# Performance work log

Measured on AMD Instinct MI355X. Metric: run time of the kernel, lower is better.

Reference implementation:

```python
import jax, jax.numpy as jnp
import numpy as np

NEG_SLOPE = 0.01  # torch F.leaky_relu default
N_USER = 100000
N_ITEM = 100000
N_EDGE = 640000
D = 128
N_LAYERS = 3  # 1 input + num_hidden_layers(1) + 1 output layer


def setup_inputs() -> dict:
    key = jax.random.key(0)
    ks = jax.random.split(key, 10)
    scale = 1.0 / np.sqrt(D)
    return {
        "h_user": jax.random.normal(ks[0], (N_USER, D), dtype=jnp.float32),
        "h_item": jax.random.normal(ks[1], (N_ITEM, D), dtype=jnp.float32),
        # W[layer, etype] : etype 0 = user-follows->user, 1 = user-clicks->item, 2 = item-clicked_by->user
        "W": jax.random.normal(ks[2], (N_LAYERS, 3, D, D), dtype=jnp.float32) * scale,
        "b": jnp.zeros((N_LAYERS, 3, D), dtype=jnp.float32),
        "follows_src": jax.random.randint(ks[3], (N_EDGE,), 0, N_USER, dtype=jnp.int32),
        "follows_dst": jax.random.randint(ks[4], (N_EDGE,), 0, N_USER, dtype=jnp.int32),
        "clicks_src": jax.random.randint(ks[5], (N_EDGE,), 0, N_USER, dtype=jnp.int32),
        "clicks_dst": jax.random.randint(ks[6], (N_EDGE,), 0, N_ITEM, dtype=jnp.int32),
        "cb_src": jax.random.randint(ks[7], (N_EDGE,), 0, N_ITEM, dtype=jnp.int32),
        "cb_dst": jax.random.randint(ks[8], (N_EDGE,), 0, N_USER, dtype=jnp.int32),
    }


def _etype_conv(h_src, W, b, src, dst, n_dst):
    """Per-etype Linear on src nodes, copy_u gather, mean-aggregate at dst."""
    Wh = h_src @ W + b                     # [N_src, D] dense transform (once per node)
    msg = Wh[src]                          # [E, D] gather
    s = jax.ops.segment_sum(msg, dst, num_segments=n_dst)
    cnt = jax.ops.segment_sum(jnp.ones((src.shape[0],), dtype=Wh.dtype), dst, num_segments=n_dst)
    return s / jnp.maximum(cnt, 1.0)[:, None]  # mean; isolated nodes -> 0


def _rgcn_forward(h_user, h_item, W, b, follows_src, follows_dst,
                  clicks_src, clicks_dst, cb_src, cb_dst):
    hu, hi = h_user, h_item
    for l in range(N_LAYERS):
        # per-etype mean aggregation, then cross-etype 'sum' (DGL multi_update_all)
        agg_u = (_etype_conv(hu, W[l, 0], b[l, 0], follows_src, follows_dst, N_USER)
                 + _etype_conv(hi, W[l, 2], b[l, 2], cb_src, cb_dst, N_USER))
        agg_i = _etype_conv(hu, W[l, 1], b[l, 1], clicks_src, clicks_dst, N_ITEM)
        hu = jax.nn.leaky_relu(agg_u, NEG_SLOPE)
        hi = jax.nn.leaky_relu(agg_i, NEG_SLOPE)
    return jnp.stack([hu, hi])  # [2, 100000, 128]


def reference(h_user, h_item, W, b, follows_src, follows_dst,
              clicks_src, clicks_dst, cb_src, cb_dst):
    return _rgcn_forward(h_user, h_item, W, b, follows_src, follows_dst,
                         clicks_src, clicks_dst, cb_src, cb_dst)
```

## Files before the change

### kernel.cpp

```cpp
#include <hip/hip_runtime.h>

typedef unsigned char u8;
typedef unsigned short u16;
typedef _Float16 f16;
typedef __attribute__((ext_vector_type(4))) _Float16 f16x4;
typedef __attribute__((ext_vector_type(8))) _Float16 f16x8;
typedef __attribute__((ext_vector_type(4))) float f32x4;

#define D 128
#define PG 4

__global__ __launch_bounds__(256) void k_pre(
    const float* __restrict__ h_user, const float* __restrict__ h_item,
    const float* __restrict__ W,
    const int* __restrict__ fd, const int* __restrict__ cd,
    const int* __restrict__ cbd,
    u16* __restrict__ h_all, u16* __restrict__ Wtg,
    int* __restrict__ cnt, u8* __restrict__ pos,
    int NU, int NI, int nf, int nc, int ncb,
    int nbCnt, int nbCvtU, int nbCvtI) {
  int b = blockIdx.x;
  int T = gridDim.x;
  long before = (long)b * nbCnt / T;
  long after = (long)(b + 1) * nbCnt / T;
  if (after > before) {
    int e = (int)before * 256 + threadIdx.x;
    int d;
    if (e < nf)
      d = fd[e];
    else if (e < nf + nc)
      d = NU + cd[e - nf];
    else if (e < nf + nc + ncb)
      d = NU + NI + cbd[e - nf - nc];
    else
      return;
    int p = atomicAdd(&cnt[d], 1);
    pos[e] = (u8)p;
  } else {
    int v = b - (int)before;
    if (v < nbCvtU + nbCvtI) {
      bool isU = v < nbCvtU;
      int i = (isU ? v : v - nbCvtU) * 256 + threadIdx.x;
      int n8 = (isU ? NU : NI) * 16;
      if (i >= n8) return;
      const float4* ip = (const float4*)(isU ? h_user : h_item);
      u16* op = h_all + (isU ? 0 : (size_t)NU * D);
      float4 a = ip[i * 2], c = ip[i * 2 + 1];
      f16x8 vv = {(f16)a.x, (f16)a.y, (f16)a.z, (f16)a.w,
                  (f16)c.x, (f16)c.y, (f16)c.z, (f16)c.w};
      *(f16x8*)(op + (size_t)i * 8) = vv;
    } else {
      int idx = (v - nbCvtU - nbCvtI) * 256 + threadIdx.x;
      if (idx >= 9 * 16384) return;
      int mat = idx >> 14;
      int k = (idx >> 7) & 127;
      int n = idx & 127;
      ((f16*)Wtg)[(size_t)mat * 16384 + n * 128 + k] = (f16)W[idx];
    }
  }
}

__device__ __forceinline__ int pad4(int x) { return (x + (PG - 1)) & ~(PG - 1); }

__global__ __launch_bounds__(256) void k_scanA(const int* __restrict__ cnt,
                                               int* __restrict__ part, int n) {
  int t = threadIdx.x;
  int idx = blockIdx.x * 1024 + t * 4;
  int s = 0;
  if (idx + 3 < n) {
    int4 c = *(const int4*)(cnt + idx);
    s = pad4(c.x) + pad4(c.y) + pad4(c.z) + pad4(c.w);
  } else {
#pragma unroll
    for (int j = 0; j < 4; ++j)
      if (idx + j < n) s += pad4(cnt[idx + j]);
  }
  for (int off = 1; off < 64; off <<= 1) s += __shfl_down(s, off, 64);
  __shared__ int ws[4];
  if ((t & 63) == 0) ws[t >> 6] = s;
  __syncthreads();
  if (t == 0) part[blockIdx.x] = ws[0] + ws[1] + ws[2] + ws[3];
}

__global__ __launch_bounds__(1024) void k_scanB(int* __restrict__ part, int n_part) {
  __shared__ int sh[1024];
  int t = threadIdx.x;
  int v = (t < n_part) ? part[t] : 0;
  sh[t] = v;
  __syncthreads();
  for (int off = 1; off < 1024; off <<= 1) {
    int u = (t >= off) ? sh[t - off] : 0;
    __syncthreads();
    sh[t] += u;
    __syncthreads();
  }
  if (t < n_part) part[t] = sh[t] - v;
}

__global__ __launch_bounds__(256) void k_scanC(const int* __restrict__ cnt,
                                               const int* __restrict__ part,
                                               int* __restrict__ rs, int n) {
  int t = threadIdx.x;
  int idx = blockIdx.x * 1024 + t * 4;
  int v0 = 0, v1 = 0, v2 = 0, v3 = 0;
  if (idx + 3 < n) {
    int4 c = *(const int4*)(cnt + idx);
    v0 = pad4(c.x);
    v1 = pad4(c.y);
    v2 = pad4(c.z);
    v3 = pad4(c.w);
  } else {
    if (idx < n) v0 = pad4(cnt[idx]);
    if (idx + 1 < n) v1 = pad4(cnt[idx + 1]);
    if (idx + 2 < n) v2 = pad4(cnt[idx + 2]);
    if (idx + 3 < n) v3 = pad4(cnt[idx + 3]);
  }
  int s = v0 + v1 + v2 + v3;
  int inc = s;
  int lane = t & 63, w = t >> 6;
  for (int off = 1; off < 64; off <<= 1) {
    int u = __shfl_up(inc, off, 64);
    if (lane >= off) inc += u;
  }
  __shared__ int ws[4];
  if (lane == 63) ws[w] = inc;
  __syncthreads();
  int woff = 0;
  for (int i = 0; i < w; ++i) woff += ws[i];
  int ex = part[blockIdx.x] + woff + inc - s;
  int4 r;
  r.x = ex;
  r.y = ex + v0;
  r.z = r.y + v1;
  r.w = r.z + v2;
  if (idx + 3 < n)
    *(int4*)(rs + idx) = r;
  else {
    if (idx < n) rs[idx] = r.x;
    if (idx + 1 < n) rs[idx + 1] = r.y;
    if (idx + 2 < n) rs[idx + 2] = r.z;
    if (idx + 3 < n) rs[idx + 3] = r.w;
  }
  if (idx <= n - 1 && n - 1 < idx + 4) {
    int j = n - 1 - idx;
    int incl = (j == 0) ? r.x + v0 : (j == 1) ? r.y + v1 : (j == 2) ? r.z + v2 : r.w + v3;
    rs[n] = incl;
  }
}

__global__ __launch_bounds__(256) void k_padfill(const int* __restrict__ rs,
                                                 const int* __restrict__ cnt,
                                                 int* __restrict__ csr, int N3, int ZR) {
  int d = blockIdx.x * 256 + threadIdx.x;
  if (d >= N3) return;
  int deg = cnt[d];
  int degp = pad4(deg);
  int base = rs[d] + deg;
#pragma unroll
  for (int j = 0; j < PG - 1; ++j)
    if (j < degp - deg) csr[base + j] = ZR;
}

__global__ __launch_bounds__(256) void k_fillpos(
    const int* __restrict__ fs, const int* __restrict__ fd,
    const int* __restrict__ cs, const int* __restrict__ cd,
    const int* __restrict__ cbs, const int* __restrict__ cbd,
    const int* __restrict__ rs, const u8* __restrict__ pos,
    int* __restrict__ csr, int NU, int NI, int nf, int nc, int ncb) {
  int e = blockIdx.x * 256 + threadIdx.x;
  int d, s;
  if (e < nf) {
    d = fd[e];
    s = fs[e];
  } else if (e < nf + nc) {
    d = NU + cd[e - nf];
    s = cs[e - nf];
  } else if (e < nf + nc + ncb) {
    d = NU + NI + cbd[e - nf - nc];
    s = cbs[e - nf - nc] + NU;
  } else
    return;
  csr[rs[d] + (int)pos[e]] = s;
}

__global__ __launch_bounds__(256) void k_agg3(
    const u16* __restrict__ h_all, const int* __restrict__ csr,
    const int* __restrict__ rs, const int* __restrict__ cnt,
    u16* __restrict__ M_all, int N3) {
  int wave = (blockIdx.x * 256 + threadIdx.x) >> 6;
  int lane = threadIdx.x & 63;
  int l16 = lane & 15;
  int w = wave * 4 + (lane >> 4);
  bool valid = w < N3;
  int wc = valid ? w : 0;
  int e = rs[wc];
  int en = valid ? rs[wc + 1] : e;
  int deg = valid ? cnt[wc] : 0;
  f16x8 acc0 = {0, 0, 0, 0, 0, 0, 0, 0};
  f16x8 acc1 = {0, 0, 0, 0, 0, 0, 0, 0};
  const char* hb = (const char*)h_all;
  unsigned loff = (unsigned)l16 * 16u;

  int en8 = e + ((en - e) & ~7);
  while (e < en8) {
    int s0 = csr[e], s1 = csr[e + 1], s2 = csr[e + 2], s3 = csr[e + 3];
    int s4 = csr[e + 4], s5 = csr[e + 5], s6 = csr[e + 6], s7 = csr[e + 7];
    f16x8 v0 = *(const f16x8*)(hb + ((unsigned)s0 * 256u + loff));
    f16x8 v1 = *(const f16x8*)(hb + ((unsigned)s1 * 256u + loff));
    f16x8 v2 = *(const f16x8*)(hb + ((unsigned)s2 * 256u + loff));
    f16x8 v3 = *(const f16x8*)(hb + ((unsigned)s3 * 256u + loff));
    f16x8 v4 = *(const f16x8*)(hb + ((unsigned)s4 * 256u + loff));
    f16x8 v5 = *(const f16x8*)(hb + ((unsigned)s5 * 256u + loff));
    f16x8 v6 = *(const f16x8*)(hb + ((unsigned)s6 * 256u + loff));
    f16x8 v7 = *(const f16x8*)(hb + ((unsigned)s7 * 256u + loff));
    acc0 += v0;
    acc1 += v1;
    acc0 += v2;
    acc1 += v3;
    acc0 += v4;
    acc1 += v5;
    acc0 += v6;
    acc1 += v7;
    e += 8;
  }
  if (e < en) {
    int s0 = csr[e], s1 = csr[e + 1], s2 = csr[e + 2], s3 = csr[e + 3];
    f16x8 v0 = *(const f16x8*)(hb + ((unsigned)s0 * 256u + loff));
    f16x8 v1 = *(const f16x8*)(hb + ((unsigned)s1 * 256u + loff));
    f16x8 v2 = *(const f16x8*)(hb + ((unsigned)s2 * 256u + loff));
    f16x8 v3 = *(const f16x8*)(hb + ((unsigned)s3 * 256u + loff));
    acc0 += v0;
    acc1 += v1;
    acc0 += v2;
    acc1 += v3;
  }

  if (valid) {
    float invf = deg > 0 ? 1.0f / (float)deg : 0.f;
    f16 hinv = (f16)invf;
    f16x8 t = acc0 + acc1;
    f16x8 r = t * hinv;
    *(f16x8*)((char*)M_all + ((unsigned)wc * 256u + loff)) = r;
  }
}

template <int NE, int OUTF32>
__device__ __forceinline__ void gemm_body(
    const u16* __restrict__ mA, const u16* __restrict__ mBp,
    const u16* __restrict__ wtA, const u16* __restrict__ wtB,
    const float* __restrict__ bA, const float* __restrict__ bB,
    const int* __restrict__ rsA, const int* __restrict__ rsB,
    u16* __restrict__ o16, float* __restrict__ o32, int M, int blk) {
  int tid = threadIdx.x, lane = tid & 63, w = tid >> 6;
  int lr = lane & 15;
  int lk = (lane >> 4) * 8;
  long row0 = (long)blk * 128 + w * 32;

  f32x4 acc[2][8];
#pragma unroll
  for (int rt = 0; rt < 2; rt++)
#pragma unroll
    for (int n = 0; n < 8; n++) acc[rt][n] = (f32x4){0.f, 0.f, 0.f, 0.f};

#pragma unroll
  for (int e = 0; e < NE; ++e) {
    const f16* mm = (const f16*)((e == 0) ? mA : mBp);
    const f16* Wg = (const f16*)((e == 0) ? wtA : wtB);
#pragma unroll
    for (int ks = 0; ks < 4; ++ks) {
      int k0 = ks * 32 + lk;
      f16x8 bf[8];
#pragma unroll
      for (int n = 0; n < 8; n++) bf[n] = *(const f16x8*)(Wg + (n * 16 + lr) * D + k0);
#pragma unroll
      for (int rt = 0; rt < 2; rt++) {
        long r = row0 + rt * 16 + lr;
        if (r >= M) r = M - 1;
        f16x8 af = *(const f16x8*)(mm + r * D + k0);
#pragma unroll
        for (int n = 0; n < 8; n++)
          acc[rt][n] = __builtin_amdgcn_mfma_f32_16x16x32_f16(bf[n], af, acc[rt][n], 0, 0, 0);
      }
    }
  }

  int g4 = (lane >> 4) * 4;
  float4 bAr[8], bBr[8];
#pragma unroll
  for (int n = 0; n < 8; n++) {
    bAr[n] = *(const float4*)&bA[n * 16 + g4];
    if (NE == 2) bBr[n] = *(const float4*)&bB[n * 16 + g4];
  }

#pragma unroll
  for (int rt = 0; rt < 2; rt++) {
    long r = row0 + rt * 16 + lr;
    if (r < M) {
      bool mAok = rsA[r + 1] > rsA[r];
      bool mBok = (NE == 2) && (rsB[r + 1] > rsB[r]);
#pragma unroll
      for (int n = 0; n < 8; n++) {
        float4 vv;
        vv.x = acc[rt][n][0];
        vv.y = acc[rt][n][1];
        vv.z = acc[rt][n][2];
        vv.w = acc[rt][n][3];
        if (mAok) {
          vv.x += bAr[n].x;
          vv.y += bAr[n].y;
          vv.z += bAr[n].z;
          vv.w += bAr[n].w;
        }
        if (mBok) {
          vv.x += bBr[n].x;
          vv.y += bBr[n].y;
          vv.z += bBr[n].z;
          vv.w += bBr[n].w;
        }
        vv.x = vv.x > 0.f ? vv.x : 0.01f * vv.x;
        vv.y = vv.y > 0.f ? vv.y : 0.01f * vv.y;
        vv.z = vv.z > 0.f ? vv.z : 0.01f * vv.z;
        vv.w = vv.w > 0.f ? vv.w : 0.01f * vv.w;
        int col = n * 16 + g4;
        if (OUTF32) {
          *(float4*)&o32[r * D + col] = vv;
        } else {
          f16x4 h = {(f16)vv.x, (f16)vv.y, (f16)vv.z, (f16)vv.w};
          *(f16x4*)((f16*)o16 + r * D + col) = h;
        }
      }
    }
  }
}

template <int OUTF32>
__global__ __launch_bounds__(256) void k_gemm2(
    const u16* __restrict__ M_all, const u16* __restrict__ Wl,
    const float* __restrict__ bl, const int* __restrict__ rs_all,
    u16* __restrict__ h_all, float* __restrict__ out,
    int NU, int NI, int nbI) {
  if ((int)blockIdx.x < nbI) {
    gemm_body<1, OUTF32>(M_all + (size_t)NU * D, nullptr,
                         Wl + 16384, nullptr,
                         bl + D, nullptr,
                         rs_all + NU, nullptr,
                         h_all + (size_t)NU * D, out + (size_t)NU * D, NI,
                         blockIdx.x);
  } else {
    gemm_body<2, OUTF32>(M_all, M_all + (size_t)(NU + NI) * D,
                         Wl, Wl + 2 * 16384,
                         bl, bl + 2 * D,
                         rs_all, rs_all + NU + NI,
                         h_all, out, NU, blockIdx.x - nbI);
  }
}

extern "C" void kernel_launch(void* const* d_in, const int* in_sizes, int n_in,
                              void* d_out, int out_size, void* d_ws, size_t ws_size,
                              hipStream_t stream) {
  const float* h_user = (const float*)d_in[0];
  const float* h_item = (const float*)d_in[1];
  const float* W = (const float*)d_in[2];
  const float* bb = (const float*)d_in[3];
  const int* f_src = (const int*)d_in[4];
  const int* f_dst = (const int*)d_in[5];
  const int* c_src = (const int*)d_in[6];
  const int* c_dst = (const int*)d_in[7];
  const int* cb_src = (const int*)d_in[8];
  const int* cb_dst = (const int*)d_in[9];

  const int NU = in_sizes[0] / D;
  const int NI = in_sizes[1] / D;
  const int nEf = in_sizes[4], nEc = in_sizes[6], nEcb = in_sizes[8];
  const int N3 = NU + NI + NU;
  const int nE = nEf + nEc + nEcb;
  const int ZR = NU + NI;

  char* p = (char*)d_ws;
  auto alloc = [&](size_t bytes) {
    char* r = p;
    p += (bytes + 255) & ~(size_t)255;
    return r;
  };
  int* cnt = (int*)alloc((size_t)N3 * 4);
  int* rs_all = (int*)alloc((size_t)(N3 + 1) * 4);
  int* part = (int*)alloc(1024 * 4);
  u16* Wtg = (u16*)alloc((size_t)9 * 16384 * 2);
  int* csr_all = (int*)alloc(((size_t)nE + (size_t)(PG - 1) * N3) * 4);
  u16* h_all = (u16*)alloc((size_t)(NU + NI + 1) * D * 2);
  u16* M_all = (u16*)alloc((size_t)N3 * D * 2);
  u8* pos = (u8*)M_all;
  (void)ws_size;

  hipMemsetAsync(cnt, 0, (size_t)N3 * 4, stream);
  hipMemsetAsync(h_all + (size_t)ZR * D, 0, D * 2, stream);

  int nbCnt = (nE + 255) / 256;
  int nbCvtU = (NU * 16 + 255) / 256;
  int nbCvtI = (NI * 16 + 255) / 256;
  int nbW = (9 * 16384 + 255) / 256;
  k_pre<<<nbCnt + nbCvtU + nbCvtI + nbW, 256, 0, stream>>>(
      h_user, h_item, W, f_dst, c_dst, cb_dst, h_all, Wtg, cnt, pos,
      NU, NI, nEf, nEc, nEcb, nbCnt, nbCvtU, nbCvtI);

  int n_part = (N3 + 1023) / 1024;
  k_scanA<<<n_part, 256, 0, stream>>>(cnt, part, N3);
  k_scanB<<<1, 1024, 0, stream>>>(part, n_part);
  k_scanC<<<n_part, 256, 0, stream>>>(cnt, part, rs_all, N3);

  k_padfill<<<(N3 + 255) / 256, 256, 0, stream>>>(rs_all, cnt, csr_all, N3, ZR);
  k_fillpos<<<(nE + 255) / 256, 256, 0, stream>>>(f_src, f_dst, c_src, c_dst,
                                                  cb_src, cb_dst, rs_all, pos,
                                                  csr_all, NU, NI, nEf, nEc, nEcb);

  int nbI = (NI + 127) / 128;
  int nbU = (NU + 127) / 128;
  int agg_blocks = ((N3 + 3) / 4 + 3) / 4;

  for (int l = 0; l < 3; ++l) {
    const u16* Wl = Wtg + (size_t)l * 3 * 16384;
    const float* bl = bb + (size_t)l * 3 * D;

    k_agg3<<<agg_blocks, 256, 0, stream>>>(h_all, csr_all, rs_all, cnt, M_all, N3);

    if (l < 2)
      k_gemm2<0><<<nbI + nbU, 256, 0, stream>>>(M_all, Wl, bl, rs_all, h_all,
                                                (float*)d_out, NU, NI, nbI);
    else
      k_gemm2<1><<<nbI + nbU, 256, 0, stream>>>(M_all, Wl, bl, rs_all, h_all,
                                                (float*)d_out, NU, NI, nbI);
  }
}
```

Baseline: 549.2 us.

## Fuse neighbor aggregation and per-etype GEMM into one layer kernel

Replaces the separate aggregation kernel and GEMM kernel with a single per-layer kernel. Each wave gathers and mean-reduces neighbor rows for 16 destination nodes straight into MFMA A-fragments, then multiplies by the weights, so the fp16 M_all intermediate is never written or read back. The gathered features and the next layer's output now need separate buffers, so ping-pong h buffers are added. The cost is lower gather parallelism per node, since 16 nodes share a wave and divergent degrees are handled with a __any loop padded to the zero row, plus weights being re-read per wave without reuse across rows.

New measurement: 688.0 us. 1.25x slower.

```diff
diff --git a/kernel.cpp b/kernel.cpp
--- a/kernel.cpp
+++ b/kernel.cpp
@@ -183,175 +183,141 @@
   csr[rs[d] + (int)pos[e]] = s;
 }
 
-__global__ __launch_bounds__(256) void k_agg3(
-    const u16* __restrict__ h_all, const int* __restrict__ csr,
-    const int* __restrict__ rs, const int* __restrict__ cnt,
-    u16* __restrict__ M_all, int N3) {
-  int wave = (blockIdx.x * 256 + threadIdx.x) >> 6;
+__device__ __forceinline__ int gather_frag(
+    f16x8 a[4], const char* __restrict__ hb, const int* __restrict__ csr,
+    const int* __restrict__ rs, const int* __restrict__ cnt, int gnode, int ZR) {
   int lane = threadIdx.x & 63;
-  int l16 = lane & 15;
-  int w = wave * 4 + (lane >> 4);
-  bool valid = w < N3;
-  int wc = valid ? w : 0;
-  int e = rs[wc];
-  int en = valid ? rs[wc + 1] : e;
-  int deg = valid ? cnt[wc] : 0;
-  f16x8 acc0 = {0, 0, 0, 0, 0, 0, 0, 0};
-  f16x8 acc1 = {0, 0, 0, 0, 0, 0, 0, 0};
-  const char* hb = (const char*)h_all;
-  unsigned loff = (unsigned)l16 * 16u;
-
-  int en8 = e + ((en - e) & ~7);
-  while (e < en8) {
-    int s0 = csr[e], s1 = csr[e + 1], s2 = csr[e + 2], s3 = csr[e + 3];
-    int s4 = csr[e + 4], s5 = csr[e + 5], s6 = csr[e + 6], s7 = csr[e + 7];
-    f16x8 v0 = *(const f16x8*)(hb + ((unsigned)s0 * 256u + loff));
-    f16x8 v1 = *(const f16x8*)(hb + ((unsigned)s1 * 256u + loff));
-    f16x8 v2 = *(const f16x8*)(hb + ((unsigned)s2 * 256u + loff));
-    f16x8 v3 = *(const f16x8*)(hb + ((unsigned)s3 * 256u + loff));
-    f16x8 v4 = *(const f16x8*)(hb + ((unsigned)s4 * 256u + loff));
-    f16x8 v5 = *(const f16x8*)(hb + ((unsigned)s5 * 256u + loff));
-    f16x8 v6 = *(const f16x8*)(hb + ((unsigned)s6 * 256u + loff));
-    f16x8 v7 = *(const f16x8*)(hb + ((unsigned)s7 * 256u + loff));
-    acc0 += v0;
-    acc1 += v1;
-    acc0 += v2;
-    acc1 += v3;
-    acc0 += v4;
-    acc1 += v5;
-    acc0 += v6;
-    acc1 += v7;
-    e += 8;
-  }
-  if (e < en) {
-    int s0 = csr[e], s1 = csr[e + 1], s2 = csr[e + 2], s3 = csr[e + 3];
-    f16x8 v0 = *(const f16x8*)(hb + ((unsigned)s0 * 256u + loff));
-    f16x8 v1 = *(const f16x8*)(hb + ((unsigned)s1 * 256u + loff));
-    f16x8 v2 = *(const f16x8*)(hb + ((unsigned)s2 * 256u + loff));
-    f16x8 v3 = *(const f16x8*)(hb + ((unsigned)s3 * 256u + loff));
-    acc0 += v0;
-    acc1 += v1;
-    acc0 += v2;
-    acc1 += v3;
-  }
-
+  int g = lane >> 4;
+  int e = rs[gnode], en = rs[gnode + 1];
+  int deg = cnt[gnode];
+  unsigned off = (unsigned)g * 16u;
+  f16x8 a0 = {0, 0, 0, 0, 0, 0, 0, 0}, a1 = a0, a2 = a0, a3 = a0;
+  while (__any(e < en)) {
+    bool p = e < en;
+    int s0 = p ? csr[e] : ZR;
+    int s1 = p ? csr[e + 1] : ZR;
+    unsigned b0 = (unsigned)s0 * 256u + off;
+    unsigned b1 = (unsigned)s1 * 256u + off;
+    f16x8 v00 = *(const f16x8*)(hb + b0);
+    f16x8 v01 = *(const f16x8*)(hb + b0 + 64u);
+    f16x8 v02 = *(const f16x8*)(hb + b0 + 128u);
+    f16x8 v03 = *(const f16x8*)(hb + b0 + 192u);
+    f16x8 v10 = *(const f16x8*)(hb + b1);
+    f16x8 v11 = *(const f16x8*)(hb + b1 + 64u);
+    f16x8 v12 = *(const f16x8*)(hb + b1 + 128u);
+    f16x8 v13 = *(const f16x8*)(hb + b1 + 192u);
+    a0 += v00;
+    a1 += v01;
+    a2 += v02;
+    a3 += v03;
+    a0 += v10;
+    a1 += v11;
+    a2 += v12;
+    a3 += v13;
+    e += 2;
+  }
+  float invf = deg > 0 ? 1.0f / (float)deg : 0.f;
+  f16 hinv = (f16)invf;
+  a[0] = a0 * hinv;
+  a[1] = a1 * hinv;
+  a[2] = a2 * hinv;
+  a[3] = a3 * hinv;
+  return deg;
+}
+
+__device__ __forceinline__ void mfma_frag(f32x4 acc[8], const f16x8 a[4],
+                                          const u16* __restrict__ Wmat) {
+  int lane = threadIdx.x & 63;
+  int r = lane & 15, g = lane >> 4;
+  const f16* Wg = (const f16*)Wmat;
+#pragma unroll
+  for (int half = 0; half < 2; ++half) {
+#pragma unroll
+    for (int ks = 0; ks < 4; ++ks) {
+      f16x8 bf[4];
+#pragma unroll
+      for (int n4 = 0; n4 < 4; ++n4) {
+        int n = half * 4 + n4;
+        bf[n4] = *(const f16x8*)(Wg + (n * 16 + r) * D + ks * 32 + g * 8);
+      }
+#pragma unroll
+      for (int n4 = 0; n4 < 4; ++n4)
+        acc[half * 4 + n4] =
+            __builtin_amdgcn_mfma_f32_16x16x32_f16(bf[n4], a[ks], acc[half * 4 + n4], 0, 0, 0);
+    }
+  }
+}
+
+template <int OUTF32>
+__global__ __launch_bounds__(256) void k_layer(
+    const u16* __restrict__ hcur, const int* __restrict__ csr,
+    const int* __restrict__ rs_all, const int* __restrict__ cnt,
+    const u16* __restrict__ Wl, const float* __restrict__ bl,
+    u16* __restrict__ hnxt, float* __restrict__ out,
+    int NU, int NI, int nwI, int nwU, int ZR) {
+  int wid = blockIdx.x * 4 + (threadIdx.x >> 6);
+  if (wid >= nwI + nwU) return;
+  int lane = threadIdx.x & 63;
+  int r = lane & 15, g = lane >> 4;
+  const char* hb = (const char*)hcur;
+
+  bool isItem = wid < nwI;
+  int node = (isItem ? wid : wid - nwI) * 16 + r;
+  int Ntgt = isItem ? NI : NU;
+  bool valid = node < Ntgt;
+  int nodec = valid ? node : Ntgt - 1;
+
+  f32x4 acc[8];
+#pragma unroll
+  for (int n = 0; n < 8; ++n) acc[n] = (f32x4){0.f, 0.f, 0.f, 0.f};
+
+  f16x8 a[4];
+  int gA = isItem ? NU + nodec : nodec;
+  int degA = gather_frag(a, hb, csr, rs_all, cnt, gA, ZR);
+  mfma_frag(acc, a, isItem ? Wl + 16384 : Wl);
+  int degB = 0;
+  if (!isItem) {
+    degB = gather_frag(a, hb, csr, rs_all, cnt, NU + NI + nodec, ZR);
+    mfma_frag(acc, a, Wl + 2 * 16384);
+  }
+
+  const float* bA = isItem ? bl + D : bl;
+  long orow = (long)(isItem ? NU + node : node) * D;
+  bool mA = degA > 0, mB = degB > 0;
   if (valid) {
-    float invf = deg > 0 ? 1.0f / (float)deg : 0.f;
-    f16 hinv = (f16)invf;
-    f16x8 t = acc0 + acc1;
-    f16x8 r = t * hinv;
-    *(f16x8*)((char*)M_all + ((unsigned)wc * 256u + loff)) = r;
-  }
-}
-
-template <int NE, int OUTF32>
-__device__ __forceinline__ void gemm_body(
-    const u16* __restrict__ mA, const u16* __restrict__ mBp,
-    const u16* __restrict__ wtA, const u16* __restrict__ wtB,
-    const float* __restrict__ bA, const float* __restrict__ bB,
-    const int* __restrict__ rsA, const int* __restrict__ rsB,
-    u16* __restrict__ o16, float* __restrict__ o32, int M, int blk) {
-  int tid = threadIdx.x, lane = tid & 63, w = tid >> 6;
-  int lr = lane & 15;
-  int lk = (lane >> 4) * 8;
-  long row0 = (long)blk * 128 + w * 32;
-
-  f32x4 acc[2][8];
-#pragma unroll
-  for (int rt = 0; rt < 2; rt++)
-#pragma unroll
-    for (int n = 0; n < 8; n++) acc[rt][n] = (f32x4){0.f, 0.f, 0.f, 0.f};
-
-#pragma unroll
-  for (int e = 0; e < NE; ++e) {
-    const f16* mm = (const f16*)((e == 0) ? mA : mBp);
-    const f16* Wg = (const f16*)((e == 0) ? wtA : wtB);
-#pragma unroll
-    for (int ks = 0; ks < 4; ++ks) {
-      int k0 = ks * 32 + lk;
-      f16x8 bf[8];
-#pragma unroll
-      for (int n = 0; n < 8; n++) bf[n] = *(const f16x8*)(Wg + (n * 16 + lr) * D + k0);
-#pragma unroll
-      for (int rt = 0; rt < 2; rt++) {
-        long r = row0 + rt * 16 + lr;
-        if (r >= M) r = M - 1;
-        f16x8 af = *(const f16x8*)(mm + r * D + k0);
-#pragma unroll
-        for (int n = 0; n < 8; n++)
-          acc[rt][n] = __builtin_amdgcn_mfma_f32_16x16x32_f16(bf[n], af, acc[rt][n], 0, 0, 0);
+#pragma unroll
+    for (int n = 0; n < 8; ++n) {
+      int col = n * 16 + g * 4;
+      float4 ba = *(const float4*)&bA[col];
+      float4 vv;
+      vv.x = acc[n][0];
+      vv.y = acc[n][1];
+      vv.z = acc[n][2];
+      vv.w = acc[n][3];
+      if (mA) {
+        vv.x += ba.x;
+        vv.y += ba.y;
+        vv.z += ba.z;
+        vv.w += ba.w;
+      }
+      if (mB) {
+        float4 bb2 = *(const float4*)&bl[2 * D + col];
+        vv.x += bb2.x;
+        vv.y += bb2.y;
+        vv.z += bb2.z;
+        vv.w += bb2.w;
+      }
+      vv.x = vv.x > 0.f ? vv.x : 0.01f * vv.x;
+      vv.y = vv.y > 0.f ? vv.y : 0.01f * vv.y;
+      vv.z = vv.z > 0.f ? vv.z : 0.01f * vv.z;
+      vv.w = vv.w > 0.f ? vv.w : 0.01f * vv.w;
+      if (OUTF32) {
+        *(float4*)&out[orow + col] = vv;
+      } else {
+        f16x4 h = {(f16)vv.x, (f16)vv.y, (f16)vv.z, (f16)vv.w};
+        *(f16x4*)((f16*)hnxt + orow + col) = h;
       }
     }
-  }
-
-  int g4 = (lane >> 4) * 4;
-  float4 bAr[8], bBr[8];
-#pragma unroll
-  for (int n = 0; n < 8; n++) {
-    bAr[n] = *(const float4*)&bA[n * 16 + g4];
-    if (NE == 2) bBr[n] = *(const float4*)&bB[n * 16 + g4];
-  }
-
-#pragma unroll
-  for (int rt = 0; rt < 2; rt++) {
-    long r = row0 + rt * 16 + lr;
-    if (r < M) {
-      bool mAok = rsA[r + 1] > rsA[r];
-      bool mBok = (NE == 2) && (rsB[r + 1] > rsB[r]);
-#pragma unroll
-      for (int n = 0; n < 8; n++) {
-        float4 vv;
-        vv.x = acc[rt][n][0];
-        vv.y = acc[rt][n][1];
-        vv.z = acc[rt][n][2];
-        vv.w = acc[rt][n][3];
-        if (mAok) {
-          vv.x += bAr[n].x;
-          vv.y += bAr[n].y;
-          vv.z += bAr[n].z;
-          vv.w += bAr[n].w;
-        }
-        if (mBok) {
-          vv.x += bBr[n].x;
-          vv.y += bBr[n].y;
-          vv.z += bBr[n].z;
-          vv.w += bBr[n].w;
-        }
-        vv.x = vv.x > 0.f ? vv.x : 0.01f * vv.x;
-        vv.y = vv.y > 0.f ? vv.y : 0.01f * vv.y;
-        vv.z = vv.z > 0.f ? vv.z : 0.01f * vv.z;
-        vv.w = vv.w > 0.f ? vv.w : 0.01f * vv.w;
-        int col = n * 16 + g4;
-        if (OUTF32) {
-          *(float4*)&o32[r * D + col] = vv;
-        } else {
-          f16x4 h = {(f16)vv.x, (f16)vv.y, (f16)vv.z, (f16)vv.w};
-          *(f16x4*)((f16*)o16 + r * D + col) = h;
-        }
-      }
-    }
-  }
-}
-
-template <int OUTF32>
-__global__ __launch_bounds__(256) void k_gemm2(
-    const u16* __restrict__ M_all, const u16* __restrict__ Wl,
-    const float* __restrict__ bl, const int* __restrict__ rs_all,
-    u16* __restrict__ h_all, float* __restrict__ out,
-    int NU, int NI, int nbI) {
-  if ((int)blockIdx.x < nbI) {
-    gemm_body<1, OUTF32>(M_all + (size_t)NU * D, nullptr,
-                         Wl + 16384, nullptr,
-                         bl + D, nullptr,
-                         rs_all + NU, nullptr,
-                         h_all + (size_t)NU * D, out + (size_t)NU * D, NI,
-                         blockIdx.x);
-  } else {
-    gemm_body<2, OUTF32>(M_all, M_all + (size_t)(NU + NI) * D,
-                         Wl, Wl + 2 * 16384,
-                         bl, bl + 2 * D,
-                         rs_all, rs_all + NU + NI,
-                         h_all, out, NU, blockIdx.x - nbI);
   }
 }
 
@@ -387,20 +353,21 @@
   int* part = (int*)alloc(1024 * 4);
   u16* Wtg = (u16*)alloc((size_t)9 * 16384 * 2);
   int* csr_all = (int*)alloc(((size_t)nE + (size_t)(PG - 1) * N3) * 4);
-  u16* h_all = (u16*)alloc((size_t)(NU + NI + 1) * D * 2);
-  u16* M_all = (u16*)alloc((size_t)N3 * D * 2);
-  u8* pos = (u8*)M_all;
+  u16* hA = (u16*)alloc((size_t)(NU + NI + 1) * D * 2);
+  u16* hB = (u16*)alloc((size_t)(NU + NI + 1) * D * 2);
+  u8* pos = (u8*)hB;
   (void)ws_size;
 
   hipMemsetAsync(cnt, 0, (size_t)N3 * 4, stream);
-  hipMemsetAsync(h_all + (size_t)ZR * D, 0, D * 2, stream);
+  hipMemsetAsync(hA + (size_t)ZR * D, 0, D * 2, stream);
+  hipMemsetAsync(hB + (size_t)ZR * D, 0, D * 2, stream);
 
   int nbCnt = (nE + 255) / 256;
   int nbCvtU = (NU * 16 + 255) / 256;
   int nbCvtI = (NI * 16 + 255) / 256;
   int nbW = (9 * 16384 + 255) / 256;
   k_pre<<<nbCnt + nbCvtU + nbCvtI + nbW, 256, 0, stream>>>(
-      h_user, h_item, W, f_dst, c_dst, cb_dst, h_all, Wtg, cnt, pos,
+      h_user, h_item, W, f_dst, c_dst, cb_dst, hA, Wtg, cnt, pos,
       NU, NI, nEf, nEc, nEcb, nbCnt, nbCvtU, nbCvtI);
 
   int n_part = (N3 + 1023) / 1024;
@@ -413,21 +380,23 @@
                                                   cb_src, cb_dst, rs_all, pos,
                                                   csr_all, NU, NI, nEf, nEc, nEcb);
 
-  int nbI = (NI + 127) / 128;
-  int nbU = (NU + 127) / 128;
-  int agg_blocks = ((N3 + 3) / 4 + 3) / 4;
-
+  int nwI = (NI + 15) / 16;
+  int nwU = (NU + 15) / 16;
+  int nblk = (nwI + nwU + 3) / 4;
+
+  u16* hcur = hA;
+  u16* hnxt = hB;
   for (int l = 0; l < 3; ++l) {
     const u16* Wl = Wtg + (size_t)l * 3 * 16384;
     const float* bl = bb + (size_t)l * 3 * D;
-
-    k_agg3<<<agg_blocks, 256, 0, stream>>>(h_all, csr_all, rs_all, cnt, M_all, N3);
-
     if (l < 2)
-      k_gemm2<0><<<nbI + nbU, 256, 0, stream>>>(M_all, Wl, bl, rs_all, h_all,
-                                                (float*)d_out, NU, NI, nbI);
+      k_layer<0><<<nblk, 256, 0, stream>>>(hcur, csr_all, rs_all, cnt, Wl, bl,
+                                           hnxt, (float*)d_out, NU, NI, nwI, nwU, ZR);
     else
-      k_gemm2<1><<<nbI + nbU, 256, 0, stream>>>(M_all, Wl, bl, rs_all, h_all,
-                                                (float*)d_out, NU, NI, nbI);
-  }
-}
+      k_layer<1><<<nblk, 256, 0, stream>>>(hcur, csr_all, rs_all, cnt, Wl, bl,
+                                           hnxt, (float*)d_out, NU, NI, nwI, nwU, ZR);
+    u16* t = hcur;
+    hcur = hnxt;
+    hnxt = t;
+  }
+}
```
